# Optimization experiments

Hardware: AMD Instinct MI355X
Metric: run time of the kernel (lower is better)

Reference implementation:

```python
import jax, jax.numpy as jnp
import numpy as np

N_NODES, N_EDGES, B = 100000, 200000, 2048
ND, ED, HID, OUT, HEADS = 64, 16, 512, 512, 4

# dummy-graph topology: central node 0 -> features 1..6, plus self loops (GATv2 default)
D_SRC = jnp.array([0, 0, 0, 0, 0, 0, 0, 1, 2, 3, 4, 5, 6])
D_DST = jnp.array([1, 2, 3, 4, 5, 6, 0, 1, 2, 3, 4, 5, 6])


def setup_inputs() -> dict:
    key = jax.random.key(0)
    ks = jax.random.split(key, 40)
    p = lambda k, sh: (jax.random.normal(k, sh, dtype=jnp.float32) * 0.05)
    inp = {
        'x': jax.random.normal(ks[0], (N_NODES, ND), dtype=jnp.float32),
        'edge_index': jax.random.randint(ks[1], (2, N_EDGES), 0, N_NODES),
        'edge_attr': jax.random.normal(ks[2], (N_EDGES, ED), dtype=jnp.float32),
        'batch': jnp.sort(jax.random.randint(ks[3], (N_NODES,), 0, B)),
        'ecfp': jax.random.uniform(ks[4], (B, OUT), dtype=jnp.float32),
        'topo': jax.random.uniform(ks[5], (B, OUT), dtype=jnp.float32),
        'maccs': jax.random.uniform(ks[6], (B, OUT), dtype=jnp.float32),
        'estate': jax.random.uniform(ks[7], (B, OUT), dtype=jnp.float32),
        'rdkit2d': jax.random.normal(ks[8], (B, OUT), dtype=jnp.float32),
        'phar2d': jax.random.normal(ks[9], (B, OUT), dtype=jnp.float32),
        # GINEConv 1: nn = Linear(ND, HID); edge proj Linear(ED, ND)
        'g1_W': p(ks[10], (ND, HID)), 'g1_b': p(ks[11], (HID,)),
        'e1_W': p(ks[12], (ED, ND)), 'e1_b': p(ks[13], (ND,)),
        'bn1_g': jnp.ones((HID,), jnp.float32), 'bn1_b': jnp.zeros((HID,), jnp.float32),
        # GINEConv 2: nn = Linear(HID, OUT); edge proj Linear(ED, HID)
        'g2_W': p(ks[14], (HID, OUT)), 'g2_b': p(ks[15], (OUT,)),
        'e2_W': p(ks[16], (ED, HID)), 'e2_b': p(ks[17], (HID,)),
        'bn2_g': jnp.ones((OUT,), jnp.float32), 'bn2_b': jnp.zeros((OUT,), jnp.float32),
        # GATv2Conv 1: OUT -> HID, heads, concat=False
        'gat1_Wl': p(ks[18], (OUT, HEADS * HID)), 'gat1_bl': p(ks[19], (HEADS * HID,)),
        'gat1_Wr': p(ks[20], (OUT, HEADS * HID)), 'gat1_br': p(ks[21], (HEADS * HID,)),
        'gat1_att': p(ks[22], (HEADS, HID)), 'gat1_bias': p(ks[23], (HID,)),
        'bn3_g': jnp.ones((HID,), jnp.float32), 'bn3_b': jnp.zeros((HID,), jnp.float32),
        # GATv2Conv 2: HID -> HID
        'gat2_Wl': p(ks[24], (HID, HEADS * HID)), 'gat2_bl': p(ks[25], (HEADS * HID,)),
        'gat2_Wr': p(ks[26], (HID, HEADS * HID)), 'gat2_br': p(ks[27], (HEADS * HID,)),
        'gat2_att': p(ks[28], (HEADS, HID)), 'gat2_bias': p(ks[29], (HID,)),
        'bn4_g': jnp.ones((HID,), jnp.float32), 'bn4_b': jnp.zeros((HID,), jnp.float32),
        'fc_W': p(ks[30], (HID, 1)), 'fc_b': p(ks[31], (1,)),
    }
    return inp


def _bn_eval(h, g, b):
    # PyG BatchNorm in eval mode with fresh running stats (mean=0, var=1)
    return g * (h * (1.0 / np.sqrt(1.0 + 1e-5))) + b


def _gatv2(z, Wl, bl, Wr, br, att, bias):
    # z: [B, 7, Cin]; GATv2Conv with self-loops, concat=False (mean over heads)
    Bn, Nn, _ = z.shape
    Hh, Co = att.shape
    gl = (z @ Wl + bl).reshape(Bn, Nn, Hh, Co)  # source transform
    gr = (z @ Wr + br).reshape(Bn, Nn, Hh, Co)  # target transform
    e = jax.nn.leaky_relu(gl[:, D_SRC] + gr[:, D_DST], 0.2)  # [B, 13, H, Co]
    logits = jnp.einsum('behc,hc->beh', e, att)  # [B, 13, H]

    def seg_softmax(lg):
        m = jax.ops.segment_max(lg, D_DST, num_segments=7)
        ex = jnp.exp(lg - m[D_DST])
        s = jax.ops.segment_sum(ex, D_DST, num_segments=7)
        return ex / s[D_DST]

    alpha = jax.vmap(seg_softmax)(logits)  # [B, 13, H]
    msg = gl[:, D_SRC] * alpha[..., None]  # [B, 13, H, Co]
    out = jax.vmap(lambda mm: jax.ops.segment_sum(mm, D_DST, num_segments=7))(msg)
    return out.mean(axis=2) + bias  # [B, 7, Co]


def reference(x, edge_index, edge_attr, batch, ecfp, topo, maccs, estate, rdkit2d, phar2d,
              g1_W, g1_b, e1_W, e1_b, bn1_g, bn1_b,
              g2_W, g2_b, e2_W, e2_b, bn2_g, bn2_b,
              gat1_Wl, gat1_bl, gat1_Wr, gat1_br, gat1_att, gat1_bias, bn3_g, bn3_b,
              gat2_Wl, gat2_bl, gat2_Wr, gat2_br, gat2_att, gat2_bias, bn4_g, bn4_b,
              fc_W, fc_b):
    N = x.shape[0]
    Bg = ecfp.shape[0]
    src, dst = edge_index[0], edge_index[1]
    # GINEConv 1: msg = relu(x_j + W_e e), sum-aggr, out = Lin(x + aggr) (eps=0)
    m = jax.nn.relu(x[src] + (edge_attr @ e1_W + e1_b))
    h = (x + jax.ops.segment_sum(m, dst, num_segments=N)) @ g1_W + g1_b
    h = jax.nn.relu(_bn_eval(h, bn1_g, bn1_b))  # dropout = identity (eval)
    # GINEConv 2
    m2 = jax.nn.relu(h[src] + (edge_attr @ e2_W + e2_b))
    h2 = (h + jax.ops.segment_sum(m2, dst, num_segments=N)) @ g2_W + g2_b
    h2 = jax.nn.relu(_bn_eval(h2, bn2_g, bn2_b))
    # global mean pool
    sums = jax.ops.segment_sum(h2, batch, num_segments=Bg)
    cnts = jax.ops.segment_sum(jnp.ones((N,), h2.dtype), batch, num_segments=Bg)
    graph_out = sums / jnp.maximum(cnts, 1.0)[:, None]  # [B, OUT]
    # batched 7-node dummy graphs (node 0 = graph embedding, 1..6 = features)
    xn = jnp.stack([graph_out, ecfp, topo, maccs, estate, rdkit2d, phar2d], axis=1)
    z = _gatv2(xn, gat1_Wl, gat1_bl, gat1_Wr, gat1_br, gat1_att, gat1_bias)
    z = jax.nn.relu(_bn_eval(z, bn3_g, bn3_b))
    z = _gatv2(z, gat2_Wl, gat2_bl, gat2_Wr, gat2_br, gat2_att, gat2_bias)
    z = jax.nn.relu(_bn_eval(z, bn4_g, bn4_b))
    return z[:, 0, :] @ fc_W + fc_b  # [B, 1]
```

## Files before the change

### kernel.cpp

```cpp
#include <hip/hip_runtime.h>
#include <hip/hip_bf16.h>

#define N_NODESC 100000
#define N_EDGESC 200000
#define BG 2048
#define NDIM 64
#define EDIM 16

typedef __bf16 bf16x8 __attribute__((ext_vector_type(8)));
typedef float f32x4 __attribute__((ext_vector_type(4)));

static __device__ __forceinline__ float bn_inv() { return 0.9999950000374997f; }

static __device__ __forceinline__ float b2f(short s) {
    __hip_bfloat16 h = *(const __hip_bfloat16*)&s;
    return __bfloat162float(h);
}

__device__ __forceinline__ void gl2lds16(const void* g, void* l) {
    __builtin_amdgcn_global_load_lds(
        (const __attribute__((address_space(1))) unsigned int*)g,
        (__attribute__((address_space(3))) unsigned int*)l, 16, 0, 0);
}

__global__ void zero_f4(float4* __restrict__ p, int n4) {
    int i = blockIdx.x * 256 + threadIdx.x;
    if (i < n4) p[i] = make_float4(0.f, 0.f, 0.f, 0.f);
}
__global__ void zero_int(int* __restrict__ p, int n) {
    int i = blockIdx.x * 256 + threadIdx.x;
    if (i < n) p[i] = 0;
}
__global__ void zero_out(float* __restrict__ p, int n) {
    int i = blockIdx.x * 256 + threadIdx.x;
    if (i < n) p[i] = 0.f;
}

__global__ void hist_dst(const int* __restrict__ dst, int* __restrict__ deg) {
    int i = blockIdx.x * 256 + threadIdx.x;
    if (i < N_EDGESC) atomicAdd(&deg[dst[i]], 1);
}
__global__ void scan_bsums(const int* __restrict__ deg, int* __restrict__ bsum, int n) {
    __shared__ int ls[256];
    int b = blockIdx.x, t = threadIdx.x;
    int s = 0;
#pragma unroll
    for (int j = 0; j < 4; j++) {
        int i = b * 1024 + t * 4 + j;
        if (i < n) s += deg[i];
    }
    ls[t] = s;
    __syncthreads();
    for (int off = 128; off; off >>= 1) {
        if (t < off) ls[t] += ls[t + off];
        __syncthreads();
    }
    if (t == 0) bsum[b] = ls[0];
}
__global__ void scan_top(int* __restrict__ bsum, int nb, int* __restrict__ total) {
    if (threadIdx.x == 0) {
        int acc = 0;
        for (int i = 0; i < nb; i++) { int v = bsum[i]; bsum[i] = acc; acc += v; }
        *total = acc;
    }
}
__global__ void scan_final(const int* __restrict__ deg, const int* __restrict__ bsum,
                           int* __restrict__ rowptr, int* __restrict__ cursor, int n) {
    __shared__ int ls[256];
    int b = blockIdx.x, t = threadIdx.x;
    int v[4], s = 0;
#pragma unroll
    for (int j = 0; j < 4; j++) {
        int i = b * 1024 + t * 4 + j;
        v[j] = (i < n) ? deg[i] : 0;
        s += v[j];
    }
    ls[t] = s;
    __syncthreads();
    int run = s;
    for (int off = 1; off < 256; off <<= 1) {
        int add = (t >= off) ? ls[t - off] : 0;
        __syncthreads();
        ls[t] += add;
        __syncthreads();
    }
    int excl = ls[t] - run + bsum[b];
#pragma unroll
    for (int j = 0; j < 4; j++) {
        int i = b * 1024 + t * 4 + j;
        if (i < n) { rowptr[i] = excl; cursor[i] = excl; excl += v[j]; }
    }
}
__global__ void scatter_eid(const int* __restrict__ dst, int* __restrict__ cursor,
                            int* __restrict__ eid) {
    int e = blockIdx.x * 256 + threadIdx.x;
    if (e < N_EDGESC) {
        int p = atomicAdd(&cursor[dst[e]], 1);
        eid[p] = e;
    }
}

__global__ void transpose_w(const float* __restrict__ W, __hip_bfloat16* __restrict__ hi,
                            int K, int N) {
    __shared__ float t[64][65];
    int k0 = blockIdx.x * 64, n0 = blockIdx.y * 64;
    int tid = threadIdx.x, tx = tid & 63, ty = tid >> 6;
    for (int r = ty; r < 64; r += 4) t[r][tx] = W[(size_t)(k0 + r) * N + n0 + tx];
    __syncthreads();
    for (int r = ty; r < 64; r += 4)
        hi[(size_t)(n0 + r) * K + k0 + tx] = __float2bfloat16(t[tx][r]);
}

__global__ void concat_bias(const float* __restrict__ a, const float* __restrict__ b,
                            float* __restrict__ o) {
    int i = blockIdx.x * 256 + threadIdx.x;
    if (i < 2048) { o[i] = a[i]; o[2048 + i] = b[i]; }
}

#define G1_NPW 8
__global__ __launch_bounds__(256, 2) void gine1_gather(
    const float* __restrict__ x, const int* __restrict__ srcv, const float* __restrict__ ea,
    const float* __restrict__ e1W, const float* __restrict__ e1b,
    const int* __restrict__ rowptr, const int* __restrict__ eid,
    __hip_bfloat16* __restrict__ xin) {
    int tid = threadIdx.x;
    int wave = tid >> 6, lane = tid & 63;
    float wreg[16];
#pragma unroll
    for (int k = 0; k < 16; k++) wreg[k] = e1W[k * 64 + lane];
    float bb = e1b[lane];
    int nbase = (blockIdx.x * 4 + wave) * G1_NPW;
#pragma unroll 1
    for (int it = 0; it < G1_NPW; it++) {
        int n = nbase + it;
        if (n >= N_NODESC) return;
        float acc = x[(size_t)n * 64 + lane];
        int beg = rowptr[n], end = rowptr[n + 1];
        for (int idx = beg; idx < end; idx++) {
            int e = eid[idx], s = srcv[e];
            const float4* ef = (const float4*)(ea + (size_t)e * 16);
            float4 e0 = ef[0], e1 = ef[1], e2 = ef[2], e3 = ef[3];
            float p = bb;
            p = fmaf(e0.x, wreg[0], p);  p = fmaf(e0.y, wreg[1], p);
            p = fmaf(e0.z, wreg[2], p);  p = fmaf(e0.w, wreg[3], p);
            p = fmaf(e1.x, wreg[4], p);  p = fmaf(e1.y, wreg[5], p);
            p = fmaf(e1.z, wreg[6], p);  p = fmaf(e1.w, wreg[7], p);
            p = fmaf(e2.x, wreg[8], p);  p = fmaf(e2.y, wreg[9], p);
            p = fmaf(e2.z, wreg[10], p); p = fmaf(e2.w, wreg[11], p);
            p = fmaf(e3.x, wreg[12], p); p = fmaf(e3.y, wreg[13], p);
            p = fmaf(e3.z, wreg[14], p); p = fmaf(e3.w, wreg[15], p);
            acc += fmaxf(x[(size_t)s * 64 + lane] + p, 0.f);
        }
        xin[(size_t)n * 64 + lane] = __float2bfloat16(acc);
    }
}

#define G2_NPB 8
__global__ __launch_bounds__(256, 5) void gine2_gather(
    const __hip_bfloat16* __restrict__ h, const int* __restrict__ srcv,
    const float* __restrict__ ea, const float* __restrict__ e2W,
    const float* __restrict__ e2b, const int* __restrict__ rowptr,
    const int* __restrict__ eid, __hip_bfloat16* __restrict__ a2, int n0, int n1) {
    int tid = threadIdx.x;
    int c0 = tid * 2;
    float wreg[2][16], breg[2];
#pragma unroll
    for (int j = 0; j < 2; j++) {
        breg[j] = e2b[c0 + j];
#pragma unroll
        for (int k = 0; k < 16; k++) wreg[j][k] = e2W[k * 512 + c0 + j];
    }
    int nbase = n0 + blockIdx.x * G2_NPB;
#pragma unroll 1
    for (int it = 0; it < G2_NPB; it++) {
        int n = nbase + it;
        if (n >= n1) return;
        unsigned int hv = *(const unsigned int*)((const short*)(h + (size_t)n * 512) + c0);
        const __hip_bfloat16* hb = (const __hip_bfloat16*)&hv;
        float acc[2] = {__bfloat162float(hb[0]), __bfloat162float(hb[1])};
        int beg = rowptr[n], end = rowptr[n + 1];
        int idx = beg;
#pragma unroll 1
        for (; idx + 2 <= end; idx += 2) {
            int ei0 = eid[idx], ei1 = eid[idx + 1];
            int s0 = srcv[ei0], s1 = srcv[ei1];
            const float4* ef0 = (const float4*)(ea + (size_t)ei0 * 16);
            const float4* ef1 = (const float4*)(ea + (size_t)ei1 * 16);
            float4 a0 = ef0[0], a1 = ef0[1], a2v = ef0[2], a3 = ef0[3];
            float4 b0 = ef1[0], b1 = ef1[1], b2v = ef1[2], b3 = ef1[3];
            unsigned int sv0 = *(const unsigned int*)((const short*)(h + (size_t)s0 * 512) + c0);
            unsigned int sv1 = *(const unsigned int*)((const short*)(h + (size_t)s1 * 512) + c0);
            const __hip_bfloat16* sb0 = (const __hip_bfloat16*)&sv0;
            const __hip_bfloat16* sb1 = (const __hip_bfloat16*)&sv1;
#pragma unroll
            for (int j = 0; j < 2; j++) {
                float p = breg[j];
                p = fmaf(a0.x, wreg[j][0], p);  p = fmaf(a0.y, wreg[j][1], p);
                p = fmaf(a0.z, wreg[j][2], p);  p = fmaf(a0.w, wreg[j][3], p);
                p = fmaf(a1.x, wreg[j][4], p);  p = fmaf(a1.y, wreg[j][5], p);
                p = fmaf(a1.z, wreg[j][6], p);  p = fmaf(a1.w, wreg[j][7], p);
                p = fmaf(a2v.x, wreg[j][8], p); p = fmaf(a2v.y, wreg[j][9], p);
                p = fmaf(a2v.z, wreg[j][10], p);p = fmaf(a2v.w, wreg[j][11], p);
                p = fmaf(a3.x, wreg[j][12], p); p = fmaf(a3.y, wreg[j][13], p);
                p = fmaf(a3.z, wreg[j][14], p); p = fmaf(a3.w, wreg[j][15], p);
                acc[j] += fmaxf(__bfloat162float(sb0[j]) + p, 0.f);
                float q = breg[j];
                q = fmaf(b0.x, wreg[j][0], q);  q = fmaf(b0.y, wreg[j][1], q);
                q = fmaf(b0.z, wreg[j][2], q);  q = fmaf(b0.w, wreg[j][3], q);
                q = fmaf(b1.x, wreg[j][4], q);  q = fmaf(b1.y, wreg[j][5], q);
                q = fmaf(b1.z, wreg[j][6], q);  q = fmaf(b1.w, wreg[j][7], q);
                q = fmaf(b2v.x, wreg[j][8], q); q = fmaf(b2v.y, wreg[j][9], q);
                q = fmaf(b2v.z, wreg[j][10], q);q = fmaf(b2v.w, wreg[j][11], q);
                q = fmaf(b3.x, wreg[j][12], q); q = fmaf(b3.y, wreg[j][13], q);
                q = fmaf(b3.z, wreg[j][14], q); q = fmaf(b3.w, wreg[j][15], q);
                acc[j] += fmaxf(__bfloat162float(sb1[j]) + q, 0.f);
            }
        }
        if (idx < end) {
            int ei = eid[idx];
            int s = srcv[ei];
            const float4* ef = (const float4*)(ea + (size_t)ei * 16);
            float4 a0 = ef[0], a1 = ef[1], a2v = ef[2], a3 = ef[3];
            unsigned int sv = *(const unsigned int*)((const short*)(h + (size_t)s * 512) + c0);
            const __hip_bfloat16* sb = (const __hip_bfloat16*)&sv;
#pragma unroll
            for (int j = 0; j < 2; j++) {
                float p = breg[j];
                p = fmaf(a0.x, wreg[j][0], p);  p = fmaf(a0.y, wreg[j][1], p);
                p = fmaf(a0.z, wreg[j][2], p);  p = fmaf(a0.w, wreg[j][3], p);
                p = fmaf(a1.x, wreg[j][4], p);  p = fmaf(a1.y, wreg[j][5], p);
                p = fmaf(a1.z, wreg[j][6], p);  p = fmaf(a1.w, wreg[j][7], p);
                p = fmaf(a2v.x, wreg[j][8], p); p = fmaf(a2v.y, wreg[j][9], p);
                p = fmaf(a2v.z, wreg[j][10], p);p = fmaf(a2v.w, wreg[j][11], p);
                p = fmaf(a3.x, wreg[j][12], p); p = fmaf(a3.y, wreg[j][13], p);
                p = fmaf(a3.z, wreg[j][14], p); p = fmaf(a3.w, wreg[j][15], p);
                acc[j] += fmaxf(__bfloat162float(sb[j]) + p, 0.f);
            }
        }
        __hip_bfloat16 o[2];
        o[0] = __float2bfloat16(acc[0]);
        o[1] = __float2bfloat16(acc[1]);
        *(unsigned int*)((short*)(a2 + (size_t)(n - n0) * 512) + c0) = *(const unsigned int*)o;
    }
}

template <int MODE>
__global__ __launch_bounds__(256, 4) void mfma_gemm(
    const __hip_bfloat16* __restrict__ A, const __hip_bfloat16* __restrict__ Bhi,
    int M, int K, int N, const float* __restrict__ bias, const float* __restrict__ bng,
    const float* __restrict__ bnb, const int* __restrict__ batch,
    float* __restrict__ psum, __hip_bfloat16* __restrict__ Cout) {
    __shared__ __align__(16) short buf[16896];
    short* AsP = buf;
    short* BhP = buf + 8192;

    int nwg = gridDim.x * gridDim.y;
    int wg = blockIdx.x + gridDim.x * blockIdx.y;
    int q = nwg >> 3, r = nwg & 7;
    int xcd = wg & 7, idx = wg >> 3;
    int swz = (xcd < r) ? (xcd * (q + 1) + idx)
                        : (r * (q + 1) + (xcd - r) * q + idx);
    int bx = swz % gridDim.x, by = swz / gridDim.x;

    int r0 = by * 128;
    int n0 = bx * 128;
    int tid = threadIdx.x;
    int lane = tid & 63;
    int wv = tid >> 6;
    int wm = (wv >> 1) * 64, wn = (wv & 1) * 64;

    f32x4 acc[4][4];
#pragma unroll
    for (int i = 0; i < 4; i++)
#pragma unroll
        for (int j = 0; j < 4; j++) acc[i][j] = (f32x4){0.f, 0.f, 0.f, 0.f};

    int rowA0 = tid >> 2, cbA0 = tid & 3;
    int rowA1 = (tid + 256) >> 2;
    int gA0 = r0 + rowA0; if (gA0 >= M) gA0 = M - 1;
    int gA1 = r0 + rowA1; if (gA1 >= M) gA1 = M - 1;
    const __hip_bfloat16* pA0 = A + (size_t)gA0 * K + cbA0 * 8;
    const __hip_bfloat16* pA1 = A + (size_t)gA1 * K + cbA0 * 8;
    const __hip_bfloat16* pB0 = Bhi + (size_t)(n0 + rowA0) * K + cbA0 * 8;
    const __hip_bfloat16* pB1 = Bhi + (size_t)(n0 + rowA1) * K + cbA0 * 8;

    int fi = lane & 15, kb = (lane >> 4) * 8;
    for (int k0 = 0; k0 < K; k0 += 64) {
        __syncthreads();
#pragma unroll
        for (int hh = 0; hh < 2; hh++) {
            int kk = k0 + hh * 32;
            gl2lds16(pA0 + kk, AsP + hh * 4096 + wv * 512);
            gl2lds16(pA1 + kk, AsP + hh * 4096 + 2048 + wv * 512);
            gl2lds16(pB0 + kk, BhP + hh * 4096 + wv * 512);
            gl2lds16(pB1 + kk, BhP + hh * 4096 + 2048 + wv * 512);
        }
        __syncthreads();
#pragma unroll
        for (int ks = 0; ks < 2; ks++) {
            bf16x8 af[4], bhf[4];
#pragma unroll
            for (int mi = 0; mi < 4; mi++)
                af[mi] = *(const bf16x8*)(AsP + ks * 4096 + (wm + mi * 16 + fi) * 32 + kb);
#pragma unroll
            for (int ni = 0; ni < 4; ni++)
                bhf[ni] = *(const bf16x8*)(BhP + ks * 4096 + (wn + ni * 16 + fi) * 32 + kb);
#pragma unroll
            for (int mi = 0; mi < 4; mi++)
#pragma unroll
                for (int ni = 0; ni < 4; ni++)
                    acc[mi][ni] = __builtin_amdgcn_mfma_f32_16x16x32_bf16(
                        af[mi], bhf[ni], acc[mi][ni], 0, 0, 0);
        }
    }
    int col_l = lane & 15, quad = lane >> 4;
    if (MODE == 0 || MODE == 1) {
        __syncthreads();
#pragma unroll
        for (int mi = 0; mi < 4; mi++) {
            int rloc = wm + mi * 16 + quad * 4;
#pragma unroll
            for (int ni = 0; ni < 4; ni++) {
                int cloc = wn + ni * 16 + col_l;
                float b0 = bias[n0 + cloc];
                float g0 = 0.f, bb0 = 0.f;
                if (MODE == 1) { g0 = bng[n0 + cloc]; bb0 = bnb[n0 + cloc]; }
#pragma unroll
                for (int reg = 0; reg < 4; reg++) {
                    float v = acc[mi][ni][reg] + b0;
                    if (MODE == 1) v = fmaxf(fmaf(v * bn_inv(), g0, bb0), 0.f);
                    __hip_bfloat16 hv = __float2bfloat16(v);
                    buf[(rloc + reg) * 132 + cloc] = *(const short*)&hv;
                }
            }
        }
        __syncthreads();
#pragma unroll
        for (int p = 0; p < 16; p++) {
            int row = p * 8 + (tid >> 5);
            int grow = r0 + row;
            if (grow < M) {
                int c4 = (tid & 31) * 4;
                short4 v = *(const short4*)(buf + row * 132 + c4);
                *(short4*)(Cout + (size_t)grow * N + n0 + c4) = v;
            }
        }
    } else {
#pragma unroll
        for (int mi = 0; mi < 4; mi++) {
            int rbase = r0 + wm + mi * 16 + quad * 4;
#pragma unroll
            for (int ni = 0; ni < 4; ni++) {
                int gcol = n0 + wn + ni * 16 + col_l;
                float b0 = bias[gcol], g0 = bng[gcol], bb0 = bnb[gcol];
                float vv[4];
#pragma unroll
                for (int reg = 0; reg < 4; reg++)
                    vv[reg] = fmaxf(fmaf((acc[mi][ni][reg] + b0) * bn_inv(), g0, bb0), 0.f);
                int rtop = r0 + wm + mi * 16;
                bool uni16 = (rtop + 15 < M) && (batch[rtop] == batch[rtop + 15]);
                float vs = (vv[0] + vv[1]) + (vv[2] + vv[3]);
                if (uni16) {
                    vs += __shfl_xor(vs, 16);
                    vs += __shfl_xor(vs, 32);
                    if (quad == 0)
                        atomicAdd(&psum[(size_t)batch[rtop] * 512 + gcol], vs);
                } else if (rbase + 3 < M && batch[rbase] == batch[rbase + 3]) {
                    atomicAdd(&psum[(size_t)batch[rbase] * 512 + gcol], vs);
                } else {
#pragma unroll
                    for (int reg = 0; reg < 4; reg++) {
                        int grow = rbase + reg;
                        if (grow < M)
                            atomicAdd(&psum[(size_t)batch[grow] * 512 + gcol], vv[reg]);
                    }
                }
            }
        }
    }
}

__global__ void count_nodes(const int* __restrict__ batch, float* __restrict__ cnt) {
    int i = blockIdx.x * 256 + threadIdx.x;
    if (i < N_NODESC) atomicAdd(&cnt[batch[i]], 1.0f);
}

__global__ void build_xn(const float* __restrict__ psum, const float* __restrict__ cnt,
                         const float* __restrict__ ecfp, const float* __restrict__ topo,
                         const float* __restrict__ maccs, const float* __restrict__ estate,
                         const float* __restrict__ rdkit2d, const float* __restrict__ phar2d,
                         __hip_bfloat16* __restrict__ xn) {
    int i = blockIdx.x * 256 + threadIdx.x;
    if (i >= BG * 512) return;
    int bidx = i >> 9, c = i & 511;
    float cv = fmaxf(cnt[bidx], 1.0f);
    __hip_bfloat16* o = xn + (size_t)bidx * 7 * 512;
    o[c] = __float2bfloat16(psum[i] / cv);
    o[512 + c] = __float2bfloat16(ecfp[i]);
    o[2 * 512 + c] = __float2bfloat16(topo[i]);
    o[3 * 512 + c] = __float2bfloat16(maccs[i]);
    o[4 * 512 + c] = __float2bfloat16(estate[i]);
    o[5 * 512 + c] = __float2bfloat16(rdkit2d[i]);
    o[6 * 512 + c] = __float2bfloat16(phar2d[i]);
}

__global__ void gat_attn(const __hip_bfloat16* __restrict__ cg,
                         const float* __restrict__ att, const float* __restrict__ bias,
                         const float* __restrict__ bng, const float* __restrict__ bnb,
                         __hip_bfloat16* __restrict__ zout) {
    int b = blockIdx.x;
    int tid = threadIdx.x;
    int wave = tid >> 6, lane = tid & 63;
    __shared__ float logits[13][4];
    __shared__ float alpha[13][4];
    const size_t base = (size_t)b * 7 * 4096;
    for (int p = wave; p < 52; p += 4) {
        int e = p >> 2, hh = p & 3;
        int se = (e < 7) ? 0 : (e - 6);
        int de = (e < 6) ? (e + 1) : ((e == 6) ? 0 : (e - 6));
        const short* glp = (const short*)(cg + base + (size_t)se * 4096 + hh * 512) + lane * 8;
        const short* grp = (const short*)(cg + base + (size_t)de * 4096 + 2048 + hh * 512) + lane * 8;
        short4 gl0 = ((const short4*)glp)[0], gl1 = ((const short4*)glp)[1];
        short4 gr0 = ((const short4*)grp)[0], gr1 = ((const short4*)grp)[1];
        const float4* ap = (const float4*)(att + hh * 512 + lane * 8);
        float4 a0 = ap[0], a1 = ap[1];
        float s = 0.f, v;
        v = b2f(gl0.x) + b2f(gr0.x); v = (v >= 0.f) ? v : 0.2f * v; s = fmaf(v, a0.x, s);
        v = b2f(gl0.y) + b2f(gr0.y); v = (v >= 0.f) ? v : 0.2f * v; s = fmaf(v, a0.y, s);
        v = b2f(gl0.z) + b2f(gr0.z); v = (v >= 0.f) ? v : 0.2f * v; s = fmaf(v, a0.z, s);
        v = b2f(gl0.w) + b2f(gr0.w); v = (v >= 0.f) ? v : 0.2f * v; s = fmaf(v, a0.w, s);
        v = b2f(gl1.x) + b2f(gr1.x); v = (v >= 0.f) ? v : 0.2f * v; s = fmaf(v, a1.x, s);
        v = b2f(gl1.y) + b2f(gr1.y); v = (v >= 0.f) ? v : 0.2f * v; s = fmaf(v, a1.y, s);
        v = b2f(gl1.z) + b2f(gr1.z); v = (v >= 0.f) ? v : 0.2f * v; s = fmaf(v, a1.z, s);
        v = b2f(gl1.w) + b2f(gr1.w); v = (v >= 0.f) ? v : 0.2f * v; s = fmaf(v, a1.w, s);
#pragma unroll
        for (int off = 32; off; off >>= 1) s += __shfl_down(s, off);
        if (lane == 0) logits[e][hh] = s;
    }
    __syncthreads();
    if (tid < 24) {
        int n = 1 + (tid >> 2), hh = tid & 3;
        float la = logits[n - 1][hh], lb = logits[6 + n][hh];
        float m = fmaxf(la, lb);
        float ea = __expf(la - m), eb = __expf(lb - m);
        float inv = 1.f / (ea + eb);
        alpha[n - 1][hh] = ea * inv;
        alpha[6 + n][hh] = eb * inv;
    } else if (tid < 28) {
        alpha[6][tid & 3] = 1.f;
    }
    __syncthreads();
    for (int u = tid; u < 7 * 128; u += 256) {
        int n = u >> 7, c4 = (u & 127) * 4;
        float v0 = 0.f, v1 = 0.f, v2 = 0.f, v3 = 0.f;
        const short* g0 = (const short*)(cg + base) + c4;
        if (n == 0) {
#pragma unroll
            for (int hh = 0; hh < 4; hh++) {
                short4 t = *(const short4*)(g0 + hh * 512);
                float a = alpha[6][hh];
                v0 = fmaf(a, b2f(t.x), v0); v1 = fmaf(a, b2f(t.y), v1);
                v2 = fmaf(a, b2f(t.z), v2); v3 = fmaf(a, b2f(t.w), v3);
            }
        } else {
            const short* gn = (const short*)(cg + base + (size_t)n * 4096) + c4;
#pragma unroll
            for (int hh = 0; hh < 4; hh++) {
                short4 t = *(const short4*)(g0 + hh * 512);
                float a = alpha[n - 1][hh];
                v0 = fmaf(a, b2f(t.x), v0); v1 = fmaf(a, b2f(t.y), v1);
                v2 = fmaf(a, b2f(t.z), v2); v3 = fmaf(a, b2f(t.w), v3);
                short4 t2 = *(const short4*)(gn + hh * 512);
                float a2 = alpha[6 + n][hh];
                v0 = fmaf(a2, b2f(t2.x), v0); v1 = fmaf(a2, b2f(t2.y), v1);
                v2 = fmaf(a2, b2f(t2.z), v2); v3 = fmaf(a2, b2f(t2.w), v3);
            }
        }
        float4 bi = *(const float4*)(bias + c4);
        float4 gg = *(const float4*)(bng + c4);
        float4 bb = *(const float4*)(bnb + c4);
        v0 = fmaxf(fmaf(fmaf(v0, 0.25f, bi.x) * bn_inv(), gg.x, bb.x), 0.f);
        v1 = fmaxf(fmaf(fmaf(v1, 0.25f, bi.y) * bn_inv(), gg.y, bb.y), 0.f);
        v2 = fmaxf(fmaf(fmaf(v2, 0.25f, bi.z) * bn_inv(), gg.z, bb.z), 0.f);
        v3 = fmaxf(fmaf(fmaf(v3, 0.25f, bi.w) * bn_inv(), gg.w, bb.w), 0.f);
        __hip_bfloat16 o[4];
        o[0] = __float2bfloat16(v0); o[1] = __float2bfloat16(v1);
        o[2] = __float2bfloat16(v2); o[3] = __float2bfloat16(v3);
        *(short4*)((short*)(zout + (size_t)b * 7 * 512) + n * 512 + c4) = *(const short4*)o;
    }
}

__global__ void final_fc(const __hip_bfloat16* __restrict__ z, const float* __restrict__ fcW,
                         const float* __restrict__ fcb, float* __restrict__ out) {
    int b = blockIdx.x * 4 + (threadIdx.x >> 6);
    int lane = threadIdx.x & 63;
    if (b >= BG) return;
    const __hip_bfloat16* row = z + (size_t)b * 7 * 512;
    float s = 0.f;
#pragma unroll
    for (int j = 0; j < 8; j++)
        s = fmaf(__bfloat162float(row[lane + j * 64]), fcW[lane + j * 64], s);
#pragma unroll
    for (int off = 32; off; off >>= 1) s += __shfl_down(s, off);
    if (lane == 0) out[b] = s + fcb[0];
}

extern "C" void kernel_launch(void* const* d_in, const int* in_sizes, int n_in,
                              void* d_out, int out_size, void* d_ws, size_t ws_size,
                              hipStream_t stream) {
    const float* x = (const float*)d_in[0];
    const int* eidx = (const int*)d_in[1];
    const float* eattr = (const float*)d_in[2];
    const int* batch = (const int*)d_in[3];
    const float* ecfp = (const float*)d_in[4];
    const float* topo = (const float*)d_in[5];
    const float* maccs = (const float*)d_in[6];
    const float* estate = (const float*)d_in[7];
    const float* rdkit2d = (const float*)d_in[8];
    const float* phar2d = (const float*)d_in[9];
    const float* g1_W = (const float*)d_in[10];
    const float* g1_b = (const float*)d_in[11];
    const float* e1_W = (const float*)d_in[12];
    const float* e1_b = (const float*)d_in[13];
    const float* bn1_g = (const float*)d_in[14];
    const float* bn1_b = (const float*)d_in[15];
    const float* g2_W = (const float*)d_in[16];
    const float* g2_b = (const float*)d_in[17];
    const float* e2_W = (const float*)d_in[18];
    const float* e2_b = (const float*)d_in[19];
    const float* bn2_g = (const float*)d_in[20];
    const float* bn2_b = (const float*)d_in[21];
    const float* gat1_Wl = (const float*)d_in[22];
    const float* gat1_bl = (const float*)d_in[23];
    const float* gat1_Wr = (const float*)d_in[24];
    const float* gat1_br = (const float*)d_in[25];
    const float* gat1_att = (const float*)d_in[26];
    const float* gat1_bias = (const float*)d_in[27];
    const float* bn3_g = (const float*)d_in[28];
    const float* bn3_b = (const float*)d_in[29];
    const float* gat2_Wl = (const float*)d_in[30];
    const float* gat2_bl = (const float*)d_in[31];
    const float* gat2_Wr = (const float*)d_in[32];
    const float* gat2_br = (const float*)d_in[33];
    const float* gat2_att = (const float*)d_in[34];
    const float* gat2_bias = (const float*)d_in[35];
    const float* bn4_g = (const float*)d_in[36];
    const float* bn4_b = (const float*)d_in[37];
    const float* fc_W = (const float*)d_in[38];
    const float* fc_b = (const float*)d_in[39];
    float* out = (float*)d_out;

    const size_t NEEDED = 194682880ull;
    if (ws_size < NEEDED) {
        zero_out<<<(BG + 255) / 256, 256, 0, stream>>>(out, BG);
        return;
    }
    char* w = (char*)d_ws;
    __hip_bfloat16* H = (__hip_bfloat16*)w;
    __hip_bfloat16* CG = (__hip_bfloat16*)w;
    __hip_bfloat16* A2 = (__hip_bfloat16*)(w + 102400000);
    __hip_bfloat16* GW12 = (__hip_bfloat16*)(w + 117440512);
    __hip_bfloat16* GW34 = (__hip_bfloat16*)(w + 121634816);
    __hip_bfloat16* Z1B = (__hip_bfloat16*)(w + 125829120);
    float* B12 = (float*)(w + 140509184);
    float* B34 = (float*)(w + 140525568);

    char* C = w + 161120256;
    __hip_bfloat16* XIN = (__hip_bfloat16*)C;
    __hip_bfloat16* XNB = (__hip_bfloat16*)C;
    __hip_bfloat16* Z2B = (__hip_bfloat16*)(C + 14680064);
    int* ROWPTR = (int*)(C + 14680064);
    int* CURSOR = (int*)(C + 15080192);
    int* EID = (int*)(C + 15480320);
    int* DEG = (int*)(C + 16280320);
    __hip_bfloat16* G1W = (__hip_bfloat16*)(C + 16680320);
    __hip_bfloat16* G2W = (__hip_bfloat16*)(C + 16745856);
    int* BSUM = (int*)(C + 17270144);

    float* PS = (float*)(w + 190480384);
    float* PC = (float*)(w + 194674688);

    const int* src = eidx;
    const int* dst = eidx + N_EDGESC;

    zero_int<<<(N_NODESC + 255) / 256, 256, 0, stream>>>(DEG, N_NODESC);
    zero_f4<<<(BG * 512 / 4 + 255) / 256, 256, 0, stream>>>((float4*)PS, BG * 512 / 4);
    zero_f4<<<(BG / 4 + 255) / 256, 256, 0, stream>>>((float4*)PC, BG / 4);
    hist_dst<<<(N_EDGESC + 255) / 256, 256, 0, stream>>>(dst, DEG);
    const int NB = (N_NODESC + 1023) / 1024;
    scan_bsums<<<NB, 256, 0, stream>>>(DEG, BSUM, N_NODESC);
    scan_top<<<1, 64, 0, stream>>>(BSUM, NB, ROWPTR + N_NODESC);
    scan_final<<<NB, 256, 0, stream>>>(DEG, BSUM, ROWPTR, CURSOR, N_NODESC);
    scatter_eid<<<(N_EDGESC + 255) / 256, 256, 0, stream>>>(dst, CURSOR, EID);

    transpose_w<<<dim3(1, 8), 256, 0, stream>>>(g1_W, G1W, 64, 512);
    transpose_w<<<dim3(8, 8), 256, 0, stream>>>(g2_W, G2W, 512, 512);

    gine1_gather<<<(N_NODESC + 4 * G1_NPW - 1) / (4 * G1_NPW), 256, 0, stream>>>(
        x, src, eattr, e1_W, e1_b, ROWPTR, EID, XIN);
    mfma_gemm<1><<<dim3(4, (N_NODESC + 127) / 128), 256, 0, stream>>>(
        XIN, G1W, N_NODESC, 64, 512, g1_b, bn1_g, bn1_b, nullptr, nullptr, H);
    count_nodes<<<(N_NODESC + 255) / 256, 256, 0, stream>>>(batch, PC);

    for (int c0n = 0; c0n < N_NODESC; c0n += 50000) {
        int c1n = c0n + 50000;
        int rows = 50000;
        gine2_gather<<<(rows + G2_NPB - 1) / G2_NPB, 256, 0, stream>>>(
            H, src, eattr, e2_W, e2_b, ROWPTR, EID, A2, c0n, c1n);
        mfma_gemm<2><<<dim3(4, (rows + 127) / 128), 256, 0, stream>>>(
            A2, G2W, rows, 512, 512, g2_b, bn2_g, bn2_b, batch + c0n, PS, nullptr);
    }

    transpose_w<<<dim3(8, 32), 256, 0, stream>>>(gat1_Wl, GW12, 512, 2048);
    transpose_w<<<dim3(8, 32), 256, 0, stream>>>(gat1_Wr, GW12 + (size_t)2048 * 512, 512, 2048);
    transpose_w<<<dim3(8, 32), 256, 0, stream>>>(gat2_Wl, GW34, 512, 2048);
    transpose_w<<<dim3(8, 32), 256, 0, stream>>>(gat2_Wr, GW34 + (size_t)2048 * 512, 512, 2048);
    concat_bias<<<8, 256, 0, stream>>>(gat1_bl, gat1_br, B12);
    concat_bias<<<8, 256, 0, stream>>>(gat2_bl, gat2_br, B34);

    build_xn<<<(BG * 512) / 256, 256, 0, stream>>>(PS, PC, ecfp, topo, maccs, estate,
                                                   rdkit2d, phar2d, XNB);
    const int MGAT = BG * 7;
    dim3 ggrid(4096 / 128, MGAT / 128);
    mfma_gemm<0><<<ggrid, 256, 0, stream>>>(XNB, GW12, MGAT, 512, 4096, B12,
                                            nullptr, nullptr, nullptr, nullptr, CG);
    gat_attn<<<BG, 256, 0, stream>>>(CG, gat1_att, gat1_bias, bn3_g, bn3_b, Z1B);
    mfma_gemm<0><<<ggrid, 256, 0, stream>>>(Z1B, GW34, MGAT, 512, 4096, B34,
                                            nullptr, nullptr, nullptr, nullptr, CG);
    gat_attn<<<BG, 256, 0, stream>>>(CG, gat2_att, gat2_bias, bn4_g, bn4_b, Z2B);
    final_fc<<<BG / 4, 256, 0, stream>>>(Z2B, fc_W, fc_b, out);
}
```

Baseline: 853.2 us.

## Overlap GINE2 gather of next chunk with GEMM of current chunk in fused kernel

Splits the second GINE layer into four 25000-node chunks and launches a fused kernel whose blocks are either GEMM tiles for the current chunk or gather blocks for the next chunk, using double-buffered A2. The aim is to overlap the latency-bound gather with the MFMA GEMM so the two kinds of work share the GPU at the same time. In exchange the gather blocks now run at a 4-wave occupancy bound and use the GEMM's shared memory allocation. There are also more launches and smaller GEMMs per chunk.

```diff
diff --git a/kernel.cpp b/kernel.cpp
--- a/kernel.cpp
+++ b/kernel.cpp
@@ -6,6 +6,7 @@
 #define BG 2048
 #define NDIM 64
 #define EDIM 16
+#define G2CH 25000
 
 typedef __bf16 bf16x8 __attribute__((ext_vector_type(8)));
 typedef float f32x4 __attribute__((ext_vector_type(4)));
@@ -156,8 +157,8 @@
 }
 
 #define G2_NPB 8
-__global__ __launch_bounds__(256, 5) void gine2_gather(
-    const __hip_bfloat16* __restrict__ h, const int* __restrict__ srcv,
+static __device__ void gather2_body(
+    int gbid, const __hip_bfloat16* __restrict__ h, const int* __restrict__ srcv,
     const float* __restrict__ ea, const float* __restrict__ e2W,
     const float* __restrict__ e2b, const int* __restrict__ rowptr,
     const int* __restrict__ eid, __hip_bfloat16* __restrict__ a2, int n0, int n1) {
@@ -170,7 +171,7 @@
 #pragma unroll
         for (int k = 0; k < 16; k++) wreg[j][k] = e2W[k * 512 + c0 + j];
     }
-    int nbase = n0 + blockIdx.x * G2_NPB;
+    int nbase = n0 + gbid * G2_NPB;
 #pragma unroll 1
     for (int it = 0; it < G2_NPB; it++) {
         int n = nbase + it;
@@ -244,23 +245,31 @@
     }
 }
 
+__global__ __launch_bounds__(256, 5) void gine2_gather(
+    const __hip_bfloat16* __restrict__ h, const int* __restrict__ srcv,
+    const float* __restrict__ ea, const float* __restrict__ e2W,
+    const float* __restrict__ e2b, const int* __restrict__ rowptr,
+    const int* __restrict__ eid, __hip_bfloat16* __restrict__ a2, int n0, int n1) {
+    gather2_body(blockIdx.x, h, srcv, ea, e2W, e2b, rowptr, eid, a2, n0, n1);
+}
+
 template <int MODE>
-__global__ __launch_bounds__(256, 4) void mfma_gemm(
+static __device__ void gemm_body(
+    int vbx, int vby, int nwgx, int nwgy,
     const __hip_bfloat16* __restrict__ A, const __hip_bfloat16* __restrict__ Bhi,
     int M, int K, int N, const float* __restrict__ bias, const float* __restrict__ bng,
     const float* __restrict__ bnb, const int* __restrict__ batch,
-    float* __restrict__ psum, __hip_bfloat16* __restrict__ Cout) {
-    __shared__ __align__(16) short buf[16896];
+    float* __restrict__ psum, __hip_bfloat16* __restrict__ Cout, short* buf) {
     short* AsP = buf;
     short* BhP = buf + 8192;
 
-    int nwg = gridDim.x * gridDim.y;
-    int wg = blockIdx.x + gridDim.x * blockIdx.y;
+    int nwg = nwgx * nwgy;
+    int wg = vbx + nwgx * vby;
     int q = nwg >> 3, r = nwg & 7;
     int xcd = wg & 7, idx = wg >> 3;
     int swz = (xcd < r) ? (xcd * (q + 1) + idx)
                         : (r * (q + 1) + (xcd - r) * q + idx);
-    int bx = swz % gridDim.x, by = swz / gridDim.x;
+    int bx = swz % nwgx, by = swz / nwgx;
 
     int r0 = by * 128;
     int n0 = bx * 128;
@@ -377,6 +386,40 @@
                 }
             }
         }
+    }
+}
+
+template <int MODE>
+__global__ __launch_bounds__(256, 4) void mfma_gemm(
+    const __hip_bfloat16* __restrict__ A, const __hip_bfloat16* __restrict__ Bhi,
+    int M, int K, int N, const float* __restrict__ bias, const float* __restrict__ bng,
+    const float* __restrict__ bnb, const int* __restrict__ batch,
+    float* __restrict__ psum, __hip_bfloat16* __restrict__ Cout) {
+    __shared__ __align__(16) short buf[16896];
+    gemm_body<MODE>(blockIdx.x, blockIdx.y, gridDim.x, gridDim.y, A, Bhi, M, K, N,
+                    bias, bng, bnb, batch, psum, Cout, buf);
+}
+
+__global__ __launch_bounds__(256, 4) void gine2_fused(
+    const __hip_bfloat16* __restrict__ h, const int* __restrict__ srcv,
+    const float* __restrict__ ea, const float* __restrict__ e2W,
+    const float* __restrict__ e2b, const int* __restrict__ rowptr,
+    const int* __restrict__ eid,
+    const __hip_bfloat16* __restrict__ A2r, __hip_bfloat16* __restrict__ A2w,
+    const __hip_bfloat16* __restrict__ G2Wp, const float* __restrict__ g2b,
+    const float* __restrict__ bng, const float* __restrict__ bnb,
+    const int* __restrict__ batchc, float* __restrict__ psum,
+    int gemmM, int gemmNwgy, int gn0, int gn1, int ngb) {
+    __shared__ __align__(16) short buf[16896];
+    int bid = blockIdx.x;
+    int q = bid / 5, r = bid % 5;
+    if (r == 2) {
+        gemm_body<2>(q & 3, q >> 2, 4, gemmNwgy, A2r, G2Wp, gemmM, 512, 512,
+                     g2b, bng, bnb, batchc, psum, nullptr, buf);
+    } else {
+        int gid = q * 4 + (r < 2 ? r : r - 1);
+        if (gid < ngb)
+            gather2_body(gid, h, srcv, ea, e2W, e2b, rowptr, eid, A2w, gn0, gn1);
     }
 }
 
@@ -602,13 +645,27 @@
         XIN, G1W, N_NODESC, 64, 512, g1_b, bn1_g, bn1_b, nullptr, nullptr, H);
     count_nodes<<<(N_NODESC + 255) / 256, 256, 0, stream>>>(batch, PC);
 
-    for (int c0n = 0; c0n < N_NODESC; c0n += 50000) {
-        int c1n = c0n + 50000;
-        int rows = 50000;
-        gine2_gather<<<(rows + G2_NPB - 1) / G2_NPB, 256, 0, stream>>>(
-            H, src, eattr, e2_W, e2_b, ROWPTR, EID, A2, c0n, c1n);
-        mfma_gemm<2><<<dim3(4, (rows + 127) / 128), 256, 0, stream>>>(
-            A2, G2W, rows, 512, 512, g2_b, bn2_g, bn2_b, batch + c0n, PS, nullptr);
+    {
+        const int GY = (G2CH + 127) / 128;
+        const int GG = 4 * GY;
+        const int NGB = (G2CH + G2_NPB - 1) / G2_NPB;
+        __hip_bfloat16* A2b[2] = {A2, A2 + (size_t)G2CH * 512};
+        gine2_gather<<<NGB, 256, 0, stream>>>(H, src, eattr, e2_W, e2_b,
+                                              ROWPTR, EID, A2b[0], 0, G2CH);
+        for (int c = 0; c < 4; c++) {
+            int c0n = c * G2CH;
+            if (c < 3) {
+                gine2_fused<<<5 * GG, 256, 0, stream>>>(
+                    H, src, eattr, e2_W, e2_b, ROWPTR, EID,
+                    A2b[c & 1], A2b[(c + 1) & 1],
+                    G2W, g2_b, bn2_g, bn2_b, batch + c0n, PS,
+                    G2CH, GY, (c + 1) * G2CH, (c + 2) * G2CH, NGB);
+            } else {
+                mfma_gemm<2><<<dim3(4, GY), 256, 0, stream>>>(
+                    A2b[c & 1], G2W, G2CH, 512, 512, g2_b, bn2_g, bn2_b,
+                    batch + c0n, PS, nullptr);
+            }
+        }
     }
 
     transpose_w<<<dim3(8, 32), 256, 0, stream>>>(gat1_Wl, GW12, 512, 2048);
```

New measurement: 974.2 us. 1.14x slower.
